# Kernel tuning notes

Hardware: AMD Instinct MI355X
Metric: run time of the kernel (lower is better)

The kernel has to match this reference:

```python
import jax, jax.numpy as jnp
import numpy as np

N_NODES = 50000
N_EDGES = 800000
D_FEAT = 128
HIDDEN = 128
BERT_DIM = 768
BATCH = 4096
MAX_ENT = 20
COMB = BERT_DIM + HIDDEN  # 896


def setup_inputs() -> dict:
    key = jax.random.key(0)
    ks = jax.random.split(key, 12)
    article_bert_embeddings = jax.random.normal(ks[0], (BATCH, BERT_DIM), dtype=jnp.float32)
    x = jax.random.normal(ks[1], (N_NODES, D_FEAT), dtype=jnp.float32)
    edge_index = jax.random.randint(ks[2], (2, N_EDGES), 0, N_NODES, dtype=jnp.int64)
    entity_map = jax.random.randint(ks[3], (BATCH, MAX_ENT), 0, N_NODES, dtype=jnp.int64)
    pad = jax.random.uniform(ks[4], (BATCH, MAX_ENT)) < 0.3
    entity_map = jnp.where(pad, jnp.int64(-1), entity_map)
    s = 1.0 / np.sqrt(D_FEAT)
    W1 = jax.random.normal(ks[5], (D_FEAT, HIDDEN), dtype=jnp.float32) * s
    b1 = jnp.zeros((HIDDEN,), dtype=jnp.float32)
    W2 = jax.random.normal(ks[6], (HIDDEN, HIDDEN), dtype=jnp.float32) * (1.0 / np.sqrt(HIDDEN))
    b2 = jnp.zeros((HIDDEN,), dtype=jnp.float32)
    fc1_w = jax.random.normal(ks[7], (COMB, COMB // 2), dtype=jnp.float32) * (1.0 / np.sqrt(COMB))
    fc1_b = jnp.zeros((COMB // 2,), dtype=jnp.float32)
    fc2_w = jax.random.normal(ks[8], (COMB // 2, 1), dtype=jnp.float32) * (1.0 / np.sqrt(COMB // 2))
    fc2_b = jnp.zeros((1,), dtype=jnp.float32)
    return dict(article_bert_embeddings=article_bert_embeddings, x=x,
                edge_index=edge_index, entity_map=entity_map,
                W1=W1, b1=b1, W2=W2, b2=b2,
                fc1_w=fc1_w, fc1_b=fc1_b, fc2_w=fc2_w, fc2_b=fc2_b)


def _gcn_norm(edge_index, n_nodes):
    # add self loops (PyG GCNConv default) and compute symmetric normalization
    loops = jnp.arange(n_nodes, dtype=edge_index.dtype)
    src = jnp.concatenate([edge_index[0], loops])
    dst = jnp.concatenate([edge_index[1], loops])
    deg = jax.ops.segment_sum(jnp.ones_like(dst, dtype=jnp.float32), dst, num_segments=n_nodes)
    dinv = jnp.where(deg > 0, jax.lax.rsqrt(deg), 0.0)
    norm = dinv[src] * dinv[dst]  # [E+N]
    return src, dst, norm


def _gcn_conv(h, W, b, src, dst, norm, n_nodes):
    h = h @ W                                   # [N, H] transform first (cheaper)
    msg = h[src] * norm[:, None]                # [E+N, H] gather
    out = jax.ops.segment_sum(msg, dst, num_segments=n_nodes)
    return out + b


def reference(article_bert_embeddings, x, edge_index, entity_map,
              W1, b1, W2, b2, fc1_w, fc1_b, fc2_w, fc2_b):
    n = x.shape[0]
    src, dst, norm = _gcn_norm(edge_index, n)
    # GNN (dropout in eval mode = identity)
    h = jax.nn.relu(_gcn_conv(x, W1, b1, src, dst, norm, n))
    h = jax.nn.relu(_gcn_conv(h, W2, b2, src, dst, norm, n))
    # ragged mean over entity lists (-1 = padding), fully vectorized
    mask = entity_map >= 0                           # [B, M]
    safe_ids = jnp.where(mask, entity_map, 0)
    gathered = h[safe_ids] * mask[..., None]         # [B, M, H]
    cnt = jnp.maximum(mask.sum(axis=1, keepdims=True).astype(h.dtype), 1.0)
    batch_gnn = gathered.sum(axis=1) / cnt           # [B, H]; rows w/ no entities stay 0
    combined = jnp.concatenate([article_bert_embeddings, batch_gnn], axis=1)
    z = jax.nn.relu(combined @ fc1_w + fc1_b)
    logits = z @ fc2_w + fc2_b
    return jax.nn.sigmoid(logits)
```

## Files before the change

kernel.cpp:

```cpp
#include <hip/hip_runtime.h>
#include <math.h>

typedef __bf16 bf16_t;
typedef __bf16 bfrag8 __attribute__((ext_vector_type(8)));
typedef float  facc4  __attribute__((ext_vector_type(4)));
typedef float  f32x2  __attribute__((ext_vector_type(2)));

#define NBUCK 512
#define BCAP  4096

__device__ inline unsigned short f2b(float x) {
    unsigned int u = __float_as_uint(x);
    unsigned int r = (u + 0x7fffu + ((u >> 16) & 1u)) >> 16;
    return (unsigned short)r;
}
__device__ inline unsigned int pack2(float lo, float hi) {
    return (unsigned int)f2b(lo) | ((unsigned int)f2b(hi) << 16);
}
__device__ inline float blo(unsigned int q) { return __uint_as_float(q << 16); }
__device__ inline float bhi(unsigned int q) { return __uint_as_float(q & 0xffff0000u); }

#if __has_builtin(__builtin_amdgcn_cvt_pk_f32_fp8) && __has_builtin(__builtin_amdgcn_cvt_pk_fp8_f32)
#define HW_FP8 1
#endif

__device__ inline f32x2 fp8pair_dec(unsigned short v) {
#ifdef HW_FP8
    return __builtin_amdgcn_cvt_pk_f32_fp8((int)(unsigned int)v, false);
#else
    f32x2 r;
    unsigned char b0 = (unsigned char)(v & 0xff), b1 = (unsigned char)(v >> 8);
    {
        int e = (b0 >> 3) & 0xf, m = b0 & 7;
        float mag = e ? ldexpf(8.f + m, e - 10) : ldexpf((float)m, -9);
        r.x = (b0 & 0x80) ? -mag : mag;
    }
    {
        int e = (b1 >> 3) & 0xf, m = b1 & 7;
        float mag = e ? ldexpf(8.f + m, e - 10) : ldexpf((float)m, -9);
        r.y = (b1 & 0x80) ? -mag : mag;
    }
    return r;
#endif
}
__device__ inline unsigned char fp8_enc(float x) {
#ifdef HW_FP8
    return (unsigned char)(__builtin_amdgcn_cvt_pk_fp8_f32(x, x, 0, false) & 0xff);
#else
    unsigned char s = (x < 0.f) ? 0x80 : 0;
    float ax = fabsf(x);
    if (!(ax > 0.f)) return s;
    if (ax >= 448.f) return s | 0x7e;
    if (ax < 0.015625f) {
        int q = (int)rintf(ax * 512.f);
        return s | (unsigned char)q;
    }
    int e; float m = frexpf(ax, &e);
    int q = (int)rintf(m * 16.f);
    int E = e - 1;
    if (q == 16) { q = 8; ++E; }
    if (E > 8) return s | 0x7e;
    return s | (unsigned char)(((E + 7) << 3) | (q - 8));
#endif
}

__device__ inline int bucket_of(int d, int N) {
    return (int)(((long long)d * NBUCK) / N);
}


__device__ inline void bin2_body(char* smem, const int* __restrict__ src,
                                 const int* __restrict__ dst,
                                 int* __restrict__ bcnt,
                                 unsigned int* __restrict__ ebuf,
                                 int E, int N, int bb) {
    unsigned int* sorted = (unsigned int*)smem;
    int* hist   = (int*)(smem + 16384);
    int* lstart = (int*)(smem + 18432);
    int* gbase  = (int*)(smem + 20480);
    int* sm     = (int*)(smem + 22528);
    int tid = threadIdx.x;
    int base = bb * 4096;
    int cnt = min(4096, E - base);
    hist[tid] = 0; hist[tid + 256] = 0;
    __syncthreads();
    unsigned int mye[16]; int myb[16];
#pragma unroll
    for (int i = 0; i < 16; ++i) {
        int idx = i * 256 + tid;
        myb[i] = -1;
        if (idx < cnt) {
            int e = base + idx;
            int s = src[e], d = dst[e];
            mye[i] = ((unsigned int)s << 16) | (unsigned int)d;
            int b = bucket_of(d, N);
            myb[i] = b;
            atomicAdd(&hist[b], 1);
        }
    }
    __syncthreads();
    int p0 = hist[2 * tid], p1 = hist[2 * tid + 1];
    sm[tid] = p0 + p1;
    __syncthreads();
    for (int off = 1; off < 256; off <<= 1) {
        int x = (tid >= off) ? sm[tid - off] : 0;
        __syncthreads();
        sm[tid] += x;
        __syncthreads();
    }
    int excl = sm[tid] - (p0 + p1);
    lstart[2 * tid] = excl;
    lstart[2 * tid + 1] = excl + p0;
    __syncthreads();
    hist[tid] = lstart[tid]; hist[tid + 256] = lstart[tid + 256];
    __syncthreads();
#pragma unroll
    for (int i = 0; i < 16; ++i) {
        if (myb[i] >= 0) {
            int pos = atomicAdd(&hist[myb[i]], 1);
            sorted[pos] = mye[i];
        }
    }
    __syncthreads();
    for (int b = tid; b < NBUCK; b += 256) {
        int c = hist[b] - lstart[b];
        gbase[b] = (c > 0) ? atomicAdd(&bcnt[b], c) : 0;
    }
    __syncthreads();
    for (int idx = tid; idx < cnt; idx += 256) {
        unsigned int v = sorted[idx];
        int b = bucket_of((int)(v & 0xffffu), N);
        ebuf[(size_t)b * BCAP + gbase[b] + (idx - lstart[b])] = v;
    }
}

__device__ inline void build2_body(char* smem, const unsigned int* __restrict__ ebuf,
                                   const int* __restrict__ bcnt,
                                   int* __restrict__ offs,
                                   float* __restrict__ dinv,
                                   unsigned short* __restrict__ csr,
                                   int N, int E, int b) {
    unsigned short* seg = (unsigned short*)smem;
    int* cnt_l  = (int*)(smem + 8192);
    int* scan_l = (int*)(smem + 8704);
    int* curs   = (int*)(smem + 9216);
    int* smr    = (int*)(smem + 9728);
    int tid = threadIdx.x;
    int part = 0;
    for (int j = tid; j < b; j += 256) part += bcnt[j];
    smr[tid] = part;
    __syncthreads();
    for (int off = 128; off > 0; off >>= 1) {
        if (tid < off) smr[tid] += smr[tid + off];
        __syncthreads();
    }
    int base = smr[0];
    int lo = (int)(((long long)b * N + NBUCK - 1) / NBUCK);
    int cnt = bcnt[b];
    int nrange = (int)(((long long)(b + 1) * N + NBUCK - 1) / NBUCK) - lo;
    if (b == 0 && tid == 0) offs[N] = E;
    if (tid < 128) cnt_l[tid] = 0;
    __syncthreads();
    for (int i = tid; i < cnt; i += 256) {
        unsigned int v = ebuf[(size_t)b * BCAP + i];
        atomicAdd(&cnt_l[(int)(v & 0xffffu) - lo], 1);
    }
    __syncthreads();
    if (tid < 128) scan_l[tid] = cnt_l[tid];
    __syncthreads();
    for (int off = 1; off < 128; off <<= 1) {
        int x = 0;
        if (tid < 128 && tid >= off) x = scan_l[tid - off];
        __syncthreads();
        if (tid < 128) scan_l[tid] += x;
        __syncthreads();
    }
    if (tid < 128) {
        int excl = scan_l[tid] - cnt_l[tid];
        curs[tid] = excl;
        if (tid < nrange) {
            offs[lo + tid] = base + excl;
            dinv[lo + tid] = rsqrtf((float)(cnt_l[tid] + 1));
        }
    }
    __syncthreads();
    for (int i = tid; i < cnt; i += 256) {
        unsigned int v = ebuf[(size_t)b * BCAP + i];
        int d = (int)(v & 0xffffu) - lo;
        int p = atomicAdd(&curs[d], 1);
        seg[p] = (unsigned short)(v >> 16);
    }
    __syncthreads();
    for (int i = tid; i < cnt; i += 256) csr[base + i] = seg[i];
}

__device__ inline void gemm1_body(char* smem, const float* __restrict__ A,
                                  const bf16_t* __restrict__ Bt,
                                  unsigned char* __restrict__ out8, int M, int bb) {
    bf16_t* As = (bf16_t*)smem;
    bf16_t* Bs = (bf16_t*)(smem + 17408);
    int t = threadIdx.x;
    int wave = t >> 6, lane = t & 63, quad = lane >> 4, l16 = lane & 15;
    int r0 = bb * 64;
#pragma unroll
    for (int i = 0; i < 4; ++i) {
        int chunk = t + i * 256;
        int row = chunk >> 4, c8 = (chunk & 15) << 3;
        int gr = r0 + row;
        float4 a0 = make_float4(0.f, 0.f, 0.f, 0.f), a1 = a0;
        if (gr < M) {
            a0 = *(const float4*)&A[(size_t)gr * 128 + c8];
            a1 = *(const float4*)&A[(size_t)gr * 128 + c8 + 4];
        }
        *(uint4*)&As[row * 136 + c8] =
            make_uint4(pack2(a0.x, a0.y), pack2(a0.z, a0.w),
                       pack2(a1.x, a1.y), pack2(a1.z, a1.w));
    }
#pragma unroll
    for (int i = 0; i < 8; ++i) {
        int chunk = t + i * 256;
        int row = chunk >> 4, c8 = (chunk & 15) << 3;
        *(uint4*)&Bs[row * 136 + c8] = *(const uint4*)&Bt[row * 128 + c8];
    }
    __syncthreads();

    facc4 acc[8];
#pragma unroll
    for (int nt = 0; nt < 8; ++nt) acc[nt] = (facc4){0.f, 0.f, 0.f, 0.f};
    int arow = (wave << 4) + l16;
#pragma unroll
    for (int ks = 0; ks < 4; ++ks) {
        int kk = ks * 32 + quad * 8;
        bfrag8 af = *(const bfrag8*)&As[arow * 136 + kk];
#pragma unroll
        for (int nt = 0; nt < 8; ++nt) {
            bfrag8 bf = *(const bfrag8*)&Bs[(nt * 16 + l16) * 136 + kk];
            acc[nt] = __builtin_amdgcn_mfma_f32_16x16x32_bf16(af, bf, acc[nt], 0, 0, 0);
        }
    }
    __syncthreads();
    unsigned char* f8t = (unsigned char*)As;
    int wrow0 = (wave << 4) + quad * 4;
#pragma unroll
    for (int r = 0; r < 4; ++r) {
        int row = wrow0 + r;
#pragma unroll
        for (int nt = 0; nt < 8; ++nt)
            f8t[row * 128 + nt * 16 + l16] = fp8_enc(acc[nt][r]);
    }
    __syncthreads();
#pragma unroll
    for (int i = 0; i < 2; ++i) {
        int idx = t + i * 256;
        int row = idx >> 3, cc = (idx & 7) << 4;
        int gr = r0 + row;
        if (gr < M) *(uint4*)&out8[(size_t)gr * 128 + cc] = *(const uint4*)&f8t[row * 128 + cc];
    }
}

__global__ __launch_bounds__(256) void k_bin_gemm(const int* __restrict__ src,
                                                  const int* __restrict__ dst,
                                                  int* __restrict__ bcnt,
                                                  unsigned int* __restrict__ ebuf,
                                                  int E, int N,
                                                  const float* __restrict__ A,
                                                  const bf16_t* __restrict__ Bt,
                                                  unsigned char* __restrict__ out8,
                                                  int nbin) {
    __shared__ __align__(16) char smem[52224];
    if ((int)blockIdx.x < nbin)
        bin2_body(smem, src, dst, bcnt, ebuf, E, N, blockIdx.x);
    else
        gemm1_body(smem, A, Bt, out8, N, blockIdx.x - nbin);
}

__global__ __launch_bounds__(256) void k_build_gemm(const unsigned int* __restrict__ ebuf,
                                                    const int* __restrict__ bcnt,
                                                    int* __restrict__ offs,
                                                    float* __restrict__ dinv,
                                                    unsigned short* __restrict__ csr,
                                                    int N, int E,
                                                    const float* __restrict__ A,
                                                    const bf16_t* __restrict__ Bt,
                                                    unsigned char* __restrict__ out8,
                                                    int tile0) {
    __shared__ __align__(16) char smem[52224];
    if ((int)blockIdx.x < NBUCK)
        build2_body(smem, ebuf, bcnt, offs, dinv, csr, N, E, blockIdx.x);
    else
        gemm1_body(smem, A, Bt, out8, N, blockIdx.x - NBUCK + tile0);
}

__global__ __launch_bounds__(256) void k_prep(const float* __restrict__ bert,
                                              unsigned int* __restrict__ bertb, int n8,
                                              const float* __restrict__ W1,
                                              unsigned short* __restrict__ w1t,
                                              const float* __restrict__ W2,
                                              unsigned short* __restrict__ w2t,
                                              const float* __restrict__ Wf,
                                              unsigned short* __restrict__ fwt,
                                              int* __restrict__ bcnt,
                                              float* __restrict__ logacc) {
    __shared__ float tile[64][65];
    int ncvt = (n8 + 255) / 256;
    int bb = blockIdx.x, tid = threadIdx.x;
    if (bb < ncvt) {
        int i = bb * 256 + tid;
        if (i >= n8) return;
        const float4* p = (const float4*)bert + (size_t)i * 2;
        float4 a = p[0], b = p[1];
        uint4 o;
        o.x = pack2(a.x, a.y);
        o.y = pack2(a.z, a.w);
        o.z = pack2(b.x, b.y);
        o.w = pack2(b.z, b.w);
        ((uint4*)bertb)[i] = o;
        return;
    }
    bb -= ncvt;
    if (bb < 128) {
        int i = bb * 256 + tid;
        const float* W = (i < 16384) ? W1 : W2;
        unsigned short* Wt = (i < 16384) ? w1t : w2t;
        int idx = i & 16383;
        int n = idx >> 7, k = idx & 127;
        Wt[idx] = f2b(W[k * 128 + n]);
        return;
    }
    bb -= 128;
    if (bb < 98) {
        int n0 = (bb % 7) * 64, k0 = (bb / 7) * 64;
#pragma unroll
        for (int i = 0; i < 16; ++i) {
            int idx = i * 256 + tid;
            int r = idx >> 6, c = idx & 63;
            tile[r][c] = Wf[(size_t)(k0 + r) * 448 + n0 + c];
        }
        __syncthreads();
#pragma unroll
        for (int i = 0; i < 16; ++i) {
            int idx = i * 256 + tid;
            int c = idx >> 6, r = idx & 63;
            fwt[(size_t)(n0 + c) * 896 + k0 + r] = f2b(tile[r][c]);
        }
        return;
    }
    if (tid < 256) { bcnt[tid] = 0; bcnt[tid + 256] = 0; }
#pragma unroll
    for (int i = 0; i < 16; ++i) logacc[i * 256 + tid] = 0.f;
}

__global__ __launch_bounds__(256) void k_gemm_nn128(const bf16_t* __restrict__ A,
                                                    const bf16_t* __restrict__ Bt,
                                                    const float* __restrict__ rs,
                                                    unsigned char* __restrict__ out8, int M) {
    __shared__ bf16_t As[64 * 136];
    __shared__ bf16_t Bs[128 * 136];
    int t = threadIdx.x;
    int wave = t >> 6, lane = t & 63, quad = lane >> 4, l16 = lane & 15;
    int r0 = blockIdx.x * 64;
#pragma unroll
    for (int i = 0; i < 4; ++i) {
        int chunk = t + i * 256;
        int row = chunk >> 4, c8 = (chunk & 15) << 3;
        int gr = r0 + row;
        uint4 v = make_uint4(0u, 0u, 0u, 0u);
        if (gr < M) v = *(const uint4*)&A[(size_t)gr * 128 + c8];
        *(uint4*)&As[row * 136 + c8] = v;
    }
#pragma unroll
    for (int i = 0; i < 8; ++i) {
        int chunk = t + i * 256;
        int row = chunk >> 4, c8 = (chunk & 15) << 3;
        *(uint4*)&Bs[row * 136 + c8] = *(const uint4*)&Bt[row * 128 + c8];
    }
    __syncthreads();

    facc4 acc[8];
#pragma unroll
    for (int nt = 0; nt < 8; ++nt) acc[nt] = (facc4){0.f, 0.f, 0.f, 0.f};
    int arow = (wave << 4) + l16;
#pragma unroll
    for (int ks = 0; ks < 4; ++ks) {
        int kk = ks * 32 + quad * 8;
        bfrag8 af = *(const bfrag8*)&As[arow * 136 + kk];
#pragma unroll
        for (int nt = 0; nt < 8; ++nt) {
            bfrag8 bf = *(const bfrag8*)&Bs[(nt * 16 + l16) * 136 + kk];
            acc[nt] = __builtin_amdgcn_mfma_f32_16x16x32_bf16(af, bf, acc[nt], 0, 0, 0);
        }
    }
    __syncthreads();
    unsigned char* f8t = (unsigned char*)As;
    int wrow0 = (wave << 4) + quad * 4;
#pragma unroll
    for (int r = 0; r < 4; ++r) {
        int row = wrow0 + r;
        float sc = rs[min(r0 + row, M - 1)];
#pragma unroll
        for (int nt = 0; nt < 8; ++nt)
            f8t[row * 128 + nt * 16 + l16] = fp8_enc(acc[nt][r] * sc);
    }
    __syncthreads();
#pragma unroll
    for (int i = 0; i < 2; ++i) {
        int idx = t + i * 256;
        int row = idx >> 3, cc = (idx & 7) << 4;
        int gr = r0 + row;
        if (gr < M) *(uint4*)&out8[(size_t)gr * 128 + cc] = *(const uint4*)&f8t[row * 128 + cc];
    }
}

__global__ __launch_bounds__(256) void k_agg_w(const unsigned short* __restrict__ hx8,
                                               const unsigned short* __restrict__ csr,
                                               const int* __restrict__ offs,
                                               const float* __restrict__ dinv,
                                               const float* __restrict__ bias,
                                               unsigned int* __restrict__ out, int N) {
    int node = blockIdx.x * 4 + (threadIdx.x >> 6);
    int lane = threadIdx.x & 63;
    if (node >= N) return;
    float di = dinv[node];
    f32x2 sf = fp8pair_dec(hx8[(size_t)node * 64 + lane]);
    float acc0 = sf.x * di, acc1 = sf.y * di;
    int s0 = offs[node], s1 = offs[node + 1];
    for (int base = s0; base < s1; base += 64) {
        int nloc = min(64, s1 - base);
        int en = 0; float dvl = 0.f;
        if (lane < nloc) { en = (int)csr[base + lane]; dvl = dinv[en]; }
        int j = 0;
        for (; j + 16 <= nloc; j += 16) {
            int sid[16]; float dv[16]; unsigned short g[16];
#pragma unroll
            for (int u = 0; u < 16; ++u) {
                sid[u] = __shfl(en, j + u, 64);
                dv[u]  = __shfl(dvl, j + u, 64);
            }
#pragma unroll
            for (int u = 0; u < 16; ++u) g[u] = hx8[(size_t)sid[u] * 64 + lane];
#pragma unroll
            for (int u = 0; u < 16; ++u) {
                f32x2 d = fp8pair_dec(g[u]);
                acc0 += d.x * dv[u]; acc1 += d.y * dv[u];
            }
        }
        for (; j + 4 <= nloc; j += 4) {
            int sid[4]; float dv[4]; unsigned short g[4];
#pragma unroll
            for (int u = 0; u < 4; ++u) {
                sid[u] = __shfl(en, j + u, 64);
                dv[u]  = __shfl(dvl, j + u, 64);
            }
#pragma unroll
            for (int u = 0; u < 4; ++u) g[u] = hx8[(size_t)sid[u] * 64 + lane];
#pragma unroll
            for (int u = 0; u < 4; ++u) {
                f32x2 d = fp8pair_dec(g[u]);
                acc0 += d.x * dv[u]; acc1 += d.y * dv[u];
            }
        }
        for (; j < nloc; ++j) {
            int srcn = __shfl(en, j, 64);
            float dv = __shfl(dvl, j, 64);
            f32x2 d = fp8pair_dec(hx8[(size_t)srcn * 64 + lane]);
            acc0 += d.x * dv; acc1 += d.y * dv;
        }
    }
    float2 bb = *(const float2*)&bias[lane * 2];
    float v0 = fmaxf(acc0 * di + bb.x, 0.f);
    float v1 = fmaxf(acc1 * di + bb.y, 0.f);
    out[(size_t)node * 64 + lane] = pack2(v0, v1);
}

__global__ __launch_bounds__(256) void k_agg_b(const unsigned short* __restrict__ hx8,
                                               const unsigned short* __restrict__ csr,
                                               const int* __restrict__ offs,
                                               const float* __restrict__ dinv,
                                               const float* __restrict__ bias,
                                               unsigned int* __restrict__ out, int N) {
    int node = blockIdx.x * 4 + (threadIdx.x >> 6);
    int lane = threadIdx.x & 63;
    if (node >= N) return;
    float di = dinv[node];
    f32x2 sf = fp8pair_dec(hx8[(size_t)node * 64 + lane]);
    float acc0 = sf.x, acc1 = sf.y;
    int s0 = offs[node], s1 = offs[node + 1];
    for (int base = s0; base < s1; base += 64) {
        int nloc = min(64, s1 - base);
        int en = 0;
        if (lane < nloc) en = (int)csr[base + lane];
        int j = 0;
        for (; j + 16 <= nloc; j += 16) {
            int sid[16]; unsigned short g[16];
#pragma unroll
            for (int u = 0; u < 16; ++u) sid[u] = __shfl(en, j + u, 64);
#pragma unroll
            for (int u = 0; u < 16; ++u) g[u] = hx8[(size_t)sid[u] * 64 + lane];
#pragma unroll
            for (int u = 0; u < 16; ++u) { f32x2 d = fp8pair_dec(g[u]); acc0 += d.x; acc1 += d.y; }
        }
        for (; j + 4 <= nloc; j += 4) {
            int sid[4]; unsigned short g[4];
#pragma unroll
            for (int u = 0; u < 4; ++u) sid[u] = __shfl(en, j + u, 64);
#pragma unroll
            for (int u = 0; u < 4; ++u) g[u] = hx8[(size_t)sid[u] * 64 + lane];
#pragma unroll
            for (int u = 0; u < 4; ++u) { f32x2 d = fp8pair_dec(g[u]); acc0 += d.x; acc1 += d.y; }
        }
        for (; j < nloc; ++j) {
            int srcn = __shfl(en, j, 64);
            f32x2 d = fp8pair_dec(hx8[(size_t)srcn * 64 + lane]);
            acc0 += d.x; acc1 += d.y;
        }
    }
    float2 bb = *(const float2*)&bias[lane * 2];
    float v0 = fmaxf(acc0 * di + bb.x, 0.f);
    float v1 = fmaxf(acc1 * di + bb.y, 0.f);
    out[(size_t)node * 64 + lane] = pack2(v0, v1);
}

__global__ __launch_bounds__(256) void k_pool_b(const unsigned int* __restrict__ h,
                                                const int* __restrict__ ent,
                                                unsigned int* __restrict__ out) {
    int r = blockIdx.x * 4 + (threadIdx.x >> 6);
    int lane = threadIdx.x & 63;
    float a0 = 0.f, a1 = 0.f;
    int cnt = 0;
#pragma unroll
    for (int m = 0; m < 20; ++m) {
        int id = ent[r * 20 + m];
        if (id >= 0) {
            unsigned int q = h[(size_t)id * 64 + lane];
            a0 += blo(q); a1 += bhi(q); cnt++;
        }
    }
    float inv = 1.f / (float)max(cnt, 1);
    out[(size_t)r * 64 + lane] = pack2(a0 * inv, a1 * inv);
}

__global__ __launch_bounds__(256) void k_mlp1_mfma(const bf16_t* __restrict__ bertb,
                                                   const bf16_t* __restrict__ gnnb,
                                                   const bf16_t* __restrict__ fwt,
                                                   const float* __restrict__ fb,
                                                   const float* __restrict__ w2,
                                                   float* __restrict__ logacc) {
    __shared__ bf16_t As[64 * 136];
    __shared__ bf16_t Bs[64 * 136];
    int t = threadIdx.x;
    int wave = t >> 6, lane = t & 63, quad = lane >> 4, l16 = lane & 15;
    int r0 = blockIdx.x * 64, c0 = blockIdx.y * 64;
    facc4 acc[4];
#pragma unroll
    for (int nt = 0; nt < 4; ++nt) acc[nt] = (facc4){0.f, 0.f, 0.f, 0.f};

    for (int ks = 0; ks < 7; ++ks) {
#pragma unroll
        for (int i = 0; i < 4; ++i) {
            int chunk = t + i * 256;
            int row = chunk >> 4, c8 = (chunk & 15) << 3;
            int gr = r0 + row;
            const bf16_t* srcp = (ks < 6) ? &bertb[(size_t)gr * 768 + ks * 128 + c8]
                                          : &gnnb[(size_t)gr * 128 + c8];
            *(uint4*)&As[row * 136 + c8] = *(const uint4*)srcp;
        }
#pragma unroll
        for (int i = 0; i < 4; ++i) {
            int chunk = t + i * 256;
            int row = chunk >> 4, c8 = (chunk & 15) << 3;
            *(uint4*)&Bs[row * 136 + c8] =
                *(const uint4*)&fwt[(size_t)(c0 + row) * 896 + ks * 128 + c8];
        }
        __syncthreads();
        int arow = (wave << 4) + l16;
#pragma unroll
        for (int sub = 0; sub < 4; ++sub) {
            int kk = sub * 32 + quad * 8;
            bfrag8 af = *(const bfrag8*)&As[arow * 136 + kk];
#pragma unroll
            for (int nt = 0; nt < 4; ++nt) {
                bfrag8 bf = *(const bfrag8*)&Bs[(nt * 16 + l16) * 136 + kk];
                acc[nt] = __builtin_amdgcn_mfma_f32_16x16x32_bf16(af, bf, acc[nt], 0, 0, 0);
            }
        }
        __syncthreads();
    }
    int rbase = r0 + (wave << 4) + quad * 4;
    float part[4] = {0.f, 0.f, 0.f, 0.f};
#pragma unroll
    for (int nt = 0; nt < 4; ++nt) {
        int col = c0 + nt * 16 + l16;
        float bb = fb[col];
        float ww = w2[col];
#pragma unroll
        for (int r = 0; r < 4; ++r)
            part[r] += fmaxf(acc[nt][r] + bb, 0.f) * ww;
    }
#pragma unroll
    for (int m = 8; m >= 1; m >>= 1) {
#pragma unroll
        for (int r = 0; r < 4; ++r) part[r] += __shfl_xor(part[r], m, 64);
    }
    if (l16 == 0) {
#pragma unroll
        for (int r = 0; r < 4; ++r) atomicAdd(&logacc[rbase + r], part[r]);
    }
}

__global__ void k_sig(const float* __restrict__ logacc, const float* __restrict__ b,
                      float* __restrict__ out, int B) {
    int i = blockIdx.x * 256 + threadIdx.x;
    if (i < B) out[i] = 1.f / (1.f + expf(-(logacc[i] + b[0])));
}

extern "C" void kernel_launch(void* const* d_in, const int* in_sizes, int n_in,
                              void* d_out, int out_size, void* d_ws, size_t ws_size,
                              hipStream_t stream) {
    const float* bert = (const float*)d_in[0];
    const float* x    = (const float*)d_in[1];
    const int*   ei   = (const int*)d_in[2];
    const int*   ent  = (const int*)d_in[3];
    const float* W1   = (const float*)d_in[4];
    const float* b1   = (const float*)d_in[5];
    const float* W2   = (const float*)d_in[6];
    const float* b2   = (const float*)d_in[7];
    const float* fc1w = (const float*)d_in[8];
    const float* fc1b = (const float*)d_in[9];
    const float* fc2w = (const float*)d_in[10];
    const float* fc2b = (const float*)d_in[11];
    float* out = (float*)d_out;

    const int N = in_sizes[1] / 128;
    const int E = in_sizes[2] / 2;
    const int B = in_sizes[0] / 768;

    const int* srcv = ei;
    const int* dstv = ei + E;

    char* wsp = (char*)d_ws;
    size_t off = 0;
    auto alloc = [&](size_t bytes) -> void* {
        void* p = wsp + off;
        off += (bytes + 255) & ~(size_t)255;
        return p;
    };
    float* dinv   = (float*)alloc((size_t)N * 4);
    int*   offs   = (int*)alloc((size_t)(N + 1) * 4);
    int*   bcnt   = (int*)alloc(NBUCK * 4);
    float* logacc = (float*)alloc((size_t)B * 4);
    unsigned int*   ebuf  = (unsigned int*)alloc((size_t)NBUCK * BCAP * 4);
    unsigned short* csr16 = (unsigned short*)alloc((size_t)E * 2);
    bf16_t* bertb = (bf16_t*)alloc((size_t)B * 768 * 2);
    bf16_t* w1t   = (bf16_t*)alloc(128 * 128 * 2);
    bf16_t* w2t   = (bf16_t*)alloc(128 * 128 * 2);
    bf16_t* fwt   = (bf16_t*)alloc((size_t)896 * 448 * 2);
    unsigned char* g8a = (unsigned char*)alloc((size_t)N * 128);
    unsigned char* g8b = (unsigned char*)alloc((size_t)N * 128);
    bf16_t* hbuf  = (bf16_t*)alloc((size_t)N * 128 * 2);
    bf16_t* gnnb  = (bf16_t*)alloc((size_t)B * 128 * 2);
    (void)ws_size; (void)n_in; (void)out_size;

    int nb8 = B * 768 / 8;
    int ncvt = (nb8 + 255) / 256;
    int nprep = ncvt + 128 + 98 + 1;
    int nbin = (E + 4095) / 4096;
    int gb = (N + 63) / 64;
    int g1a = gb / 2, g1b = gb - g1a;

    k_prep<<<nprep, 256, 0, stream>>>(bert, (unsigned int*)bertb, nb8,
                                      W1, (unsigned short*)w1t, W2, (unsigned short*)w2t,
                                      fc1w, (unsigned short*)fwt, bcnt, logacc);
    k_bin_gemm<<<nbin + g1a, 256, 0, stream>>>(srcv, dstv, bcnt, ebuf, E, N,
                                               x, w1t, g8a, nbin);
    k_build_gemm<<<NBUCK + g1b, 256, 0, stream>>>(ebuf, bcnt, offs, dinv, csr16, N, E,
                                                  x, w1t, g8a, g1a);
    k_agg_w<<<(N + 3) / 4, 256, 0, stream>>>((const unsigned short*)g8a, csr16, offs, dinv, b1,
                                             (unsigned int*)hbuf, N);
    k_gemm_nn128<<<gb, 256, 0, stream>>>(hbuf, w2t, dinv, g8b, N);
    k_agg_b<<<(N + 3) / 4, 256, 0, stream>>>((const unsigned short*)g8b, csr16, offs, dinv, b2,
                                             (unsigned int*)hbuf, N);
    k_pool_b<<<B / 4, 256, 0, stream>>>((const unsigned int*)hbuf, ent, (unsigned int*)gnnb);
    k_mlp1_mfma<<<dim3(B / 64, 7), 256, 0, stream>>>(bertb, gnnb, fwt, fc1b, fc2w, logacc);
    k_sig<<<(B + 255) / 256, 256, 0, stream>>>(logacc, fc2b, out, B);
}
```

Measured before the change: 212.6 us.

## Overlap BERT part of MLP with graph build; pre-scale features; fuse sigmoid

Splits the fc1 GEMM so the BERT-only part (K=768) runs as extra blocks inside the binning and CSR-build kernels, writing partial sums to a float z buffer. The final MLP kernel then does only the K=128 GNN part, adds z, and applies the sigmoid in the last-arriving block via a counter, which removes the separate sigmoid launch. Layer-1 features are pre-scaled by dinv in a new pass so the generic agg_b kernel can replace agg_w. This adds a scale pass, a 7MB z round-trip through memory, and an extra fp8 re-quantization step.

```diff
diff --git a/kernel.cpp b/kernel.cpp
--- a/kernel.cpp
+++ b/kernel.cpp
@@ -258,6 +258,57 @@
     }
 }
 
+__device__ inline void zmlp_body(char* smem, const bf16_t* __restrict__ bertb,
+                                 const bf16_t* __restrict__ fwt,
+                                 float* __restrict__ z, int zi) {
+    bf16_t* As = (bf16_t*)smem;
+    bf16_t* Bs = (bf16_t*)(smem + 17408);
+    int t = threadIdx.x;
+    int wave = t >> 6, lane = t & 63, quad = lane >> 4, l16 = lane & 15;
+    int rb = zi & 63, cb = zi >> 6;
+    int r0 = rb * 64, c0 = cb * 64;
+    facc4 acc[4];
+#pragma unroll
+    for (int nt = 0; nt < 4; ++nt) acc[nt] = (facc4){0.f, 0.f, 0.f, 0.f};
+    for (int ks = 0; ks < 6; ++ks) {
+#pragma unroll
+        for (int i = 0; i < 4; ++i) {
+            int chunk = t + i * 256;
+            int row = chunk >> 4, c8 = (chunk & 15) << 3;
+            *(uint4*)&As[row * 136 + c8] =
+                *(const uint4*)&bertb[(size_t)(r0 + row) * 768 + ks * 128 + c8];
+        }
+#pragma unroll
+        for (int i = 0; i < 4; ++i) {
+            int chunk = t + i * 256;
+            int row = chunk >> 4, c8 = (chunk & 15) << 3;
+            *(uint4*)&Bs[row * 136 + c8] =
+                *(const uint4*)&fwt[(size_t)(c0 + row) * 896 + ks * 128 + c8];
+        }
+        __syncthreads();
+        int arow = (wave << 4) + l16;
+#pragma unroll
+        for (int sub = 0; sub < 4; ++sub) {
+            int kk = sub * 32 + quad * 8;
+            bfrag8 af = *(const bfrag8*)&As[arow * 136 + kk];
+#pragma unroll
+            for (int nt = 0; nt < 4; ++nt) {
+                bfrag8 bf = *(const bfrag8*)&Bs[(nt * 16 + l16) * 136 + kk];
+                acc[nt] = __builtin_amdgcn_mfma_f32_16x16x32_bf16(af, bf, acc[nt], 0, 0, 0);
+            }
+        }
+        __syncthreads();
+    }
+    int rbase = r0 + (wave << 4) + quad * 4;
+#pragma unroll
+    for (int nt = 0; nt < 4; ++nt) {
+        int col = c0 + nt * 16 + l16;
+#pragma unroll
+        for (int r = 0; r < 4; ++r)
+            z[(size_t)(rbase + r) * 448 + col] = acc[nt][r];
+    }
+}
+
 __global__ __launch_bounds__(256) void k_bin_gemm(const int* __restrict__ src,
                                                   const int* __restrict__ dst,
                                                   int* __restrict__ bcnt,
@@ -266,12 +317,18 @@
                                                   const float* __restrict__ A,
                                                   const bf16_t* __restrict__ Bt,
                                                   unsigned char* __restrict__ out8,
-                                                  int nbin) {
+                                                  int nbin, int ng1,
+                                                  const bf16_t* __restrict__ bertb,
+                                                  const bf16_t* __restrict__ fwt,
+                                                  float* __restrict__ z) {
     __shared__ __align__(16) char smem[52224];
-    if ((int)blockIdx.x < nbin)
-        bin2_body(smem, src, dst, bcnt, ebuf, E, N, blockIdx.x);
+    int bb = (int)blockIdx.x;
+    if (bb < nbin)
+        bin2_body(smem, src, dst, bcnt, ebuf, E, N, bb);
+    else if (bb < nbin + ng1)
+        gemm1_body(smem, A, Bt, out8, N, bb - nbin);
     else
-        gemm1_body(smem, A, Bt, out8, N, blockIdx.x - nbin);
+        zmlp_body(smem, bertb, fwt, z, bb - nbin - ng1);
 }
 
 __global__ __launch_bounds__(256) void k_build_gemm(const unsigned int* __restrict__ ebuf,
@@ -283,12 +340,18 @@
                                                     const float* __restrict__ A,
                                                     const bf16_t* __restrict__ Bt,
                                                     unsigned char* __restrict__ out8,
-                                                    int tile0) {
+                                                    int tile0, int ng1,
+                                                    const bf16_t* __restrict__ bertb,
+                                                    const bf16_t* __restrict__ fwt,
+                                                    float* __restrict__ z, int zbase) {
     __shared__ __align__(16) char smem[52224];
-    if ((int)blockIdx.x < NBUCK)
-        build2_body(smem, ebuf, bcnt, offs, dinv, csr, N, E, blockIdx.x);
+    int bb = (int)blockIdx.x;
+    if (bb < NBUCK)
+        build2_body(smem, ebuf, bcnt, offs, dinv, csr, N, E, bb);
+    else if (bb < NBUCK + ng1)
+        gemm1_body(smem, A, Bt, out8, N, bb - NBUCK + tile0);
     else
-        gemm1_body(smem, A, Bt, out8, N, blockIdx.x - NBUCK + tile0);
+        zmlp_body(smem, bertb, fwt, z, bb - NBUCK - ng1 + zbase);
 }
 
 __global__ __launch_bounds__(256) void k_prep(const float* __restrict__ bert,
@@ -300,7 +363,8 @@
                                               const float* __restrict__ Wf,
                                               unsigned short* __restrict__ fwt,
                                               int* __restrict__ bcnt,
-                                              float* __restrict__ logacc) {
+                                              float* __restrict__ logacc,
+                                              int* __restrict__ cnt) {
     __shared__ float tile[64][65];
     int ncvt = (n8 + 255) / 256;
     int bb = blockIdx.x, tid = threadIdx.x;
@@ -346,8 +410,32 @@
         return;
     }
     if (tid < 256) { bcnt[tid] = 0; bcnt[tid + 256] = 0; }
+    if (tid < 64) cnt[tid] = 0;
 #pragma unroll
     for (int i = 0; i < 16; ++i) logacc[i * 256 + tid] = 0.f;
+}
+
+__global__ __launch_bounds__(256) void k_scale8(unsigned int* __restrict__ g8,
+                                                const float* __restrict__ dinv, int N) {
+    int i = blockIdx.x * 256 + threadIdx.x;
+    int total = N * 8;
+    if (i >= total) return;
+    int row = i >> 3;
+    float d = dinv[row];
+    uint4 v = ((const uint4*)g8)[i];
+    unsigned int w[4] = {v.x, v.y, v.z, v.w};
+#pragma unroll
+    for (int q = 0; q < 4; ++q) {
+        unsigned int x = w[q], y = 0;
+#pragma unroll
+        for (int h = 0; h < 2; ++h) {
+            f32x2 p = fp8pair_dec((unsigned short)(x >> (h * 16)));
+            y |= (unsigned int)fp8_enc(p.x * d) << (h * 16);
+            y |= (unsigned int)fp8_enc(p.y * d) << (h * 16 + 8);
+        }
+        w[q] = y;
+    }
+    ((uint4*)g8)[i] = make_uint4(w[0], w[1], w[2], w[3]);
 }
 
 __global__ __launch_bounds__(256) void k_gemm_nn128(const bf16_t* __restrict__ A,
@@ -409,67 +497,6 @@
         int gr = r0 + row;
         if (gr < M) *(uint4*)&out8[(size_t)gr * 128 + cc] = *(const uint4*)&f8t[row * 128 + cc];
     }
-}
-
-__global__ __launch_bounds__(256) void k_agg_w(const unsigned short* __restrict__ hx8,
-                                               const unsigned short* __restrict__ csr,
-                                               const int* __restrict__ offs,
-                                               const float* __restrict__ dinv,
-                                               const float* __restrict__ bias,
-                                               unsigned int* __restrict__ out, int N) {
-    int node = blockIdx.x * 4 + (threadIdx.x >> 6);
-    int lane = threadIdx.x & 63;
-    if (node >= N) return;
-    float di = dinv[node];
-    f32x2 sf = fp8pair_dec(hx8[(size_t)node * 64 + lane]);
-    float acc0 = sf.x * di, acc1 = sf.y * di;
-    int s0 = offs[node], s1 = offs[node + 1];
-    for (int base = s0; base < s1; base += 64) {
-        int nloc = min(64, s1 - base);
-        int en = 0; float dvl = 0.f;
-        if (lane < nloc) { en = (int)csr[base + lane]; dvl = dinv[en]; }
-        int j = 0;
-        for (; j + 16 <= nloc; j += 16) {
-            int sid[16]; float dv[16]; unsigned short g[16];
-#pragma unroll
-            for (int u = 0; u < 16; ++u) {
-                sid[u] = __shfl(en, j + u, 64);
-                dv[u]  = __shfl(dvl, j + u, 64);
-            }
-#pragma unroll
-            for (int u = 0; u < 16; ++u) g[u] = hx8[(size_t)sid[u] * 64 + lane];
-#pragma unroll
-            for (int u = 0; u < 16; ++u) {
-                f32x2 d = fp8pair_dec(g[u]);
-                acc0 += d.x * dv[u]; acc1 += d.y * dv[u];
-            }
-        }
-        for (; j + 4 <= nloc; j += 4) {
-            int sid[4]; float dv[4]; unsigned short g[4];
-#pragma unroll
-            for (int u = 0; u < 4; ++u) {
-                sid[u] = __shfl(en, j + u, 64);
-                dv[u]  = __shfl(dvl, j + u, 64);
-            }
-#pragma unroll
-            for (int u = 0; u < 4; ++u) g[u] = hx8[(size_t)sid[u] * 64 + lane];
-#pragma unroll
-            for (int u = 0; u < 4; ++u) {
-                f32x2 d = fp8pair_dec(g[u]);
-                acc0 += d.x * dv[u]; acc1 += d.y * dv[u];
-            }
-        }
-        for (; j < nloc; ++j) {
-            int srcn = __shfl(en, j, 64);
-            float dv = __shfl(dvl, j, 64);
-            f32x2 d = fp8pair_dec(hx8[(size_t)srcn * 64 + lane]);
-            acc0 += d.x * dv; acc1 += d.y * dv;
-        }
-    }
-    float2 bb = *(const float2*)&bias[lane * 2];
-    float v0 = fmaxf(acc0 * di + bb.x, 0.f);
-    float v1 = fmaxf(acc1 * di + bb.y, 0.f);
-    out[(size_t)node * 64 + lane] = pack2(v0, v1);
 }
 
 __global__ __launch_bounds__(256) void k_agg_b(const unsigned short* __restrict__ hx8,
@@ -539,51 +566,43 @@
     out[(size_t)r * 64 + lane] = pack2(a0 * inv, a1 * inv);
 }
 
-__global__ __launch_bounds__(256) void k_mlp1_mfma(const bf16_t* __restrict__ bertb,
-                                                   const bf16_t* __restrict__ gnnb,
-                                                   const bf16_t* __restrict__ fwt,
-                                                   const float* __restrict__ fb,
-                                                   const float* __restrict__ w2,
-                                                   float* __restrict__ logacc) {
+__global__ __launch_bounds__(256) void k_mlp2(const bf16_t* __restrict__ gnnb,
+                                              const bf16_t* __restrict__ fwt,
+                                              const float* __restrict__ z,
+                                              const float* __restrict__ fb,
+                                              const float* __restrict__ w2,
+                                              const float* __restrict__ b2s,
+                                              float* __restrict__ logacc,
+                                              int* __restrict__ cnt,
+                                              float* __restrict__ out) {
     __shared__ bf16_t As[64 * 136];
     __shared__ bf16_t Bs[64 * 136];
+    __shared__ int winflag;
     int t = threadIdx.x;
     int wave = t >> 6, lane = t & 63, quad = lane >> 4, l16 = lane & 15;
     int r0 = blockIdx.x * 64, c0 = blockIdx.y * 64;
+#pragma unroll
+    for (int i = 0; i < 4; ++i) {
+        int chunk = t + i * 256;
+        int row = chunk >> 4, c8 = (chunk & 15) << 3;
+        *(uint4*)&As[row * 136 + c8] = *(const uint4*)&gnnb[(size_t)(r0 + row) * 128 + c8];
+        *(uint4*)&Bs[row * 136 + c8] =
+            *(const uint4*)&fwt[(size_t)(c0 + row) * 896 + 768 + c8];
+    }
+    __syncthreads();
     facc4 acc[4];
 #pragma unroll
     for (int nt = 0; nt < 4; ++nt) acc[nt] = (facc4){0.f, 0.f, 0.f, 0.f};
-
-    for (int ks = 0; ks < 7; ++ks) {
-#pragma unroll
-        for (int i = 0; i < 4; ++i) {
-            int chunk = t + i * 256;
-            int row = chunk >> 4, c8 = (chunk & 15) << 3;
-            int gr = r0 + row;
-            const bf16_t* srcp = (ks < 6) ? &bertb[(size_t)gr * 768 + ks * 128 + c8]
-                                          : &gnnb[(size_t)gr * 128 + c8];
-            *(uint4*)&As[row * 136 + c8] = *(const uint4*)srcp;
-        }
-#pragma unroll
-        for (int i = 0; i < 4; ++i) {
-            int chunk = t + i * 256;
-            int row = chunk >> 4, c8 = (chunk & 15) << 3;
-            *(uint4*)&Bs[row * 136 + c8] =
-                *(const uint4*)&fwt[(size_t)(c0 + row) * 896 + ks * 128 + c8];
-        }
-        __syncthreads();
-        int arow = (wave << 4) + l16;
-#pragma unroll
-        for (int sub = 0; sub < 4; ++sub) {
-            int kk = sub * 32 + quad * 8;
-            bfrag8 af = *(const bfrag8*)&As[arow * 136 + kk];
-#pragma unroll
-            for (int nt = 0; nt < 4; ++nt) {
-                bfrag8 bf = *(const bfrag8*)&Bs[(nt * 16 + l16) * 136 + kk];
-                acc[nt] = __builtin_amdgcn_mfma_f32_16x16x32_bf16(af, bf, acc[nt], 0, 0, 0);
-            }
-        }
-        __syncthreads();
+    int arow = (wave << 4) + l16;
+#pragma unroll
+    for (int sub = 0; sub < 4; ++sub) {
+        int kk = sub * 32 + quad * 8;
+        bfrag8 af = *(const bfrag8*)&As[arow * 136 + kk];
+#pragma unroll
+        for (int nt = 0; nt < 4; ++nt) {
+            bfrag8 bf = *(const bfrag8*)&Bs[(nt * 16 + l16) * 136 + kk];
+            acc[nt] = __builtin_amdgcn_mfma_f32_16x16x32_bf16(af, bf, acc[nt], 0, 0, 0);
+        }
     }
     int rbase = r0 + (wave << 4) + quad * 4;
     float part[4] = {0.f, 0.f, 0.f, 0.f};
@@ -593,8 +612,10 @@
         float bb = fb[col];
         float ww = w2[col];
 #pragma unroll
-        for (int r = 0; r < 4; ++r)
-            part[r] += fmaxf(acc[nt][r] + bb, 0.f) * ww;
+        for (int r = 0; r < 4; ++r) {
+            float v = acc[nt][r] + z[(size_t)(rbase + r) * 448 + col];
+            part[r] += fmaxf(v + bb, 0.f) * ww;
+        }
     }
 #pragma unroll
     for (int m = 8; m >= 1; m >>= 1) {
@@ -605,12 +626,18 @@
 #pragma unroll
         for (int r = 0; r < 4; ++r) atomicAdd(&logacc[rbase + r], part[r]);
     }
-}
-
-__global__ void k_sig(const float* __restrict__ logacc, const float* __restrict__ b,
-                      float* __restrict__ out, int B) {
-    int i = blockIdx.x * 256 + threadIdx.x;
-    if (i < B) out[i] = 1.f / (1.f + expf(-(logacc[i] + b[0])));
+    __syncthreads();
+    if (t == 0) {
+        __threadfence();
+        int old = atomicAdd(&cnt[blockIdx.x], 1);
+        winflag = (old == 6);
+    }
+    __syncthreads();
+    if (winflag && t < 64) {
+        __threadfence();
+        float v = atomicAdd(&logacc[r0 + t], 0.f);
+        out[r0 + t] = 1.f / (1.f + expf(-(v + b2s[0])));
+    }
 }
 
 extern "C" void kernel_launch(void* const* d_in, const int* in_sizes, int n_in,
@@ -648,12 +675,14 @@
     int*   offs   = (int*)alloc((size_t)(N + 1) * 4);
     int*   bcnt   = (int*)alloc(NBUCK * 4);
     float* logacc = (float*)alloc((size_t)B * 4);
+    int*   cntw   = (int*)alloc(64 * 4);
     unsigned int*   ebuf  = (unsigned int*)alloc((size_t)NBUCK * BCAP * 4);
     unsigned short* csr16 = (unsigned short*)alloc((size_t)E * 2);
     bf16_t* bertb = (bf16_t*)alloc((size_t)B * 768 * 2);
     bf16_t* w1t   = (bf16_t*)alloc(128 * 128 * 2);
     bf16_t* w2t   = (bf16_t*)alloc(128 * 128 * 2);
     bf16_t* fwt   = (bf16_t*)alloc((size_t)896 * 448 * 2);
+    float*  zbuf  = (float*)alloc((size_t)B * 448 * 4);
     unsigned char* g8a = (unsigned char*)alloc((size_t)N * 128);
     unsigned char* g8b = (unsigned char*)alloc((size_t)N * 128);
     bf16_t* hbuf  = (bf16_t*)alloc((size_t)N * 128 * 2);
@@ -666,20 +695,25 @@
     int nbin = (E + 4095) / 4096;
     int gb = (N + 63) / 64;
     int g1a = gb / 2, g1b = gb - g1a;
+    int nz = (B / 64) * 7;
+    int za = nz / 2, zb = nz - za;
 
     k_prep<<<nprep, 256, 0, stream>>>(bert, (unsigned int*)bertb, nb8,
                                       W1, (unsigned short*)w1t, W2, (unsigned short*)w2t,
-                                      fc1w, (unsigned short*)fwt, bcnt, logacc);
-    k_bin_gemm<<<nbin + g1a, 256, 0, stream>>>(srcv, dstv, bcnt, ebuf, E, N,
-                                               x, w1t, g8a, nbin);
-    k_build_gemm<<<NBUCK + g1b, 256, 0, stream>>>(ebuf, bcnt, offs, dinv, csr16, N, E,
-                                                  x, w1t, g8a, g1a);
-    k_agg_w<<<(N + 3) / 4, 256, 0, stream>>>((const unsigned short*)g8a, csr16, offs, dinv, b1,
+                                      fc1w, (unsigned short*)fwt, bcnt, logacc, cntw);
+    k_bin_gemm<<<nbin + g1a + za, 256, 0, stream>>>(srcv, dstv, bcnt, ebuf, E, N,
+                                                    x, w1t, g8a, nbin, g1a,
+                                                    bertb, fwt, zbuf);
+    k_build_gemm<<<NBUCK + g1b + zb, 256, 0, stream>>>(ebuf, bcnt, offs, dinv, csr16, N, E,
+                                                       x, w1t, g8a, g1a, g1b,
+                                                       bertb, fwt, zbuf, za);
+    k_scale8<<<(N * 8 + 255) / 256, 256, 0, stream>>>((unsigned int*)g8a, dinv, N);
+    k_agg_b<<<(N + 3) / 4, 256, 0, stream>>>((const unsigned short*)g8a, csr16, offs, dinv, b1,
                                              (unsigned int*)hbuf, N);
     k_gemm_nn128<<<gb, 256, 0, stream>>>(hbuf, w2t, dinv, g8b, N);
     k_agg_b<<<(N + 3) / 4, 256, 0, stream>>>((const unsigned short*)g8b, csr16, offs, dinv, b2,
                                              (unsigned int*)hbuf, N);
     k_pool_b<<<B / 4, 256, 0, stream>>>((const unsigned int*)hbuf, ent, (unsigned int*)gnnb);
-    k_mlp1_mfma<<<dim3(B / 64, 7), 256, 0, stream>>>(bertb, gnnb, fwt, fc1b, fc2w, logacc);
-    k_sig<<<(B + 255) / 256, 256, 0, stream>>>(logacc, fc2b, out, B);
-}
+    k_mlp2<<<dim3(B / 64, 7), 256, 0, stream>>>(gnnb, fwt, zbuf, fc1b, fc2w, fc2b,
+                                                logacc, cntw, out);
+}
```

Result: no change. 214.4 us (+0.9%).
